# Kernel optimization log

Measured on AMD Instinct MI355X. Metric: run time of the kernel, lower is better.

## Reference

```python
import jax, jax.numpy as jnp
import numpy as np

B, N, NIN = 32, 128, 64
MSG_HID, MSG_OUT, N_HID, N_OUT = 256, 64, 256, 64
E = N * (N - 1)  # fully connected, no self loops


def setup_inputs() -> dict:
    key = jax.random.key(0)
    ks = jax.random.split(key, 12)

    # one-hot incidence matrices (NRI convention)
    off = np.ones((N, N), dtype=np.float32) - np.eye(N, dtype=np.float32)
    recv_idx, send_idx = np.where(off)
    eye = np.eye(N, dtype=np.float32)
    rel_rec = jnp.asarray(eye[recv_idx])    # [E, N]
    rel_send = jnp.asarray(eye[send_idx])   # [E, N]

    s = 0.05
    inp = {
        "inputs": jax.random.normal(ks[0], (B, N, NIN), jnp.float32),
        "rel_rec": rel_rec,
        "rel_send": rel_send,
        "rel_types": jax.random.uniform(ks[1], (B, E, 2), jnp.float32),
        "msg_fc1_w": jax.random.normal(ks[2], (MSG_HID, 2 * NIN), jnp.float32) * s,
        "msg_fc1_b": jnp.zeros((MSG_HID,), jnp.float32),
        "msg_fc2_w": jax.random.normal(ks[3], (MSG_OUT, MSG_HID), jnp.float32) * s,
        "msg_fc2_b": jnp.zeros((MSG_OUT,), jnp.float32),
        "out_fc1_w": jax.random.normal(ks[4], (N_HID, MSG_OUT), jnp.float32) * s,
        "out_fc1_b": jnp.zeros((N_HID,), jnp.float32),
        "out_fc2_w": jax.random.normal(ks[5], (N_HID, N_HID), jnp.float32) * s,
        "out_fc2_b": jnp.zeros((N_HID,), jnp.float32),
        "out_fc3_w": jax.random.normal(ks[6], (N_OUT, N_HID), jnp.float32) * s,
        "out_fc3_b": jnp.zeros((N_OUT,), jnp.float32),
    }
    return inp


def reference(inputs, rel_rec, rel_send, rel_types,
              msg_fc1_w, msg_fc1_b, msg_fc2_w, msg_fc2_b,
              out_fc1_w, out_fc1_b, out_fc2_w, out_fc2_b,
              out_fc3_w, out_fc3_b):
    # node2edge: gather sender / receiver node features via one-hot matmul
    senders = jnp.einsum('en,bnf->bef', rel_send, inputs)    # [B,E,NIN]
    receivers = jnp.einsum('en,bnf->bef', rel_rec, inputs)   # [B,E,NIN]
    pre_msg = jnp.concatenate([senders, receivers], axis=-1)  # [B,E,2*NIN]

    all_msgs = jnp.zeros(pre_msg.shape[:2] + (MSG_OUT,), pre_msg.dtype)
    for i in range(2):  # edge-type loop (shared weights, as in the original)
        msg = jax.nn.relu(pre_msg @ msg_fc1_w.T + msg_fc1_b)
        msg = jax.nn.relu(msg @ msg_fc2_w.T + msg_fc2_b)
        all_msgs = all_msgs + msg * rel_types[:, :, i:i + 1]

    # edge2node: scatter-add messages to receiving nodes
    agg_msgs = jnp.einsum('bem,en->bnm', all_msgs, rel_rec)   # [B,N,MSG_OUT]

    pred = jax.nn.relu(agg_msgs @ out_fc1_w.T + out_fc1_b)
    pred = jax.nn.relu(pred @ out_fc2_w.T + out_fc2_b)
    pred = pred @ out_fc3_w.T + out_fc3_b                      # [B,N,N_OUT]
    return pred
```

## Files before the change

kernel.cpp:

```cpp
#include <hip/hip_runtime.h>

#define BB 32
#define NN_ 128
#define NIN 64
#define MH 256
#define MO 64
#define NH 256
#define NO 64
#define EDGES 16256

typedef __attribute__((ext_vector_type(8))) short short8;
typedef __attribute__((ext_vector_type(4))) float f32x4;


static __device__ __forceinline__ unsigned short f2bf(float f) {
    unsigned u = __float_as_uint(f);
    u = (u + 0x7fffu + ((u >> 16) & 1u)) >> 16;
    return (unsigned short)u;
}

static __device__ __forceinline__ unsigned bf_pack(float lo, float hi) {
    return __builtin_amdgcn_perm(__float_as_uint(hi) + 0x8000u,
                                 __float_as_uint(lo) + 0x8000u, 0x07060302u);
}

__global__ __launch_bounds__(256) void prep_kernel(
    const float* __restrict__ x, const float* __restrict__ W1,
    const float* __restrict__ b1, const float* __restrict__ W2,
    const float* __restrict__ O1, const float* __restrict__ O2,
    const float* __restrict__ O3,
    unsigned short* __restrict__ psb, unsigned short* __restrict__ prb,
    unsigned short* __restrict__ w2b, unsigned short* __restrict__ o1b,
    unsigned short* __restrict__ o2b, unsigned short* __restrict__ o3b)
{
    int blk = blockIdx.x;
    int t = threadIdx.x;
    if (blk < 1024) {
        int b  = blk >> 5;
        int n0 = (blk & 31) << 2;
        __shared__ float xL[4][64];
        xL[t >> 6][t & 63] = x[((b * NN_) + n0 + (t >> 6)) * NIN + (t & 63)];
        __syncthreads();

        const float4* w1r = (const float4*)(W1 + t * (2 * NIN));
        float psv[4] = {0.f, 0.f, 0.f, 0.f};
        float prv[4];
        float bv = b1[t];
        #pragma unroll
        for (int nn = 0; nn < 4; ++nn) prv[nn] = bv;

        #pragma unroll
        for (int f4 = 0; f4 < 16; ++f4) {
            float4 w = w1r[f4];
            #pragma unroll
            for (int nn = 0; nn < 4; ++nn)
                psv[nn] += w.x * xL[nn][4*f4+0] + w.y * xL[nn][4*f4+1]
                         + w.z * xL[nn][4*f4+2] + w.w * xL[nn][4*f4+3];
        }
        #pragma unroll
        for (int f4 = 0; f4 < 16; ++f4) {
            float4 w = w1r[16 + f4];
            #pragma unroll
            for (int nn = 0; nn < 4; ++nn)
                prv[nn] += w.x * xL[nn][4*f4+0] + w.y * xL[nn][4*f4+1]
                         + w.z * xL[nn][4*f4+2] + w.w * xL[nn][4*f4+3];
        }
        #pragma unroll
        for (int nn = 0; nn < 4; ++nn) {
            int n = n0 + nn;
            prb[((b * NN_) + n) * MH + t] = f2bf(prv[nn]);
            psb[(((b * 32) + (t >> 3)) * NN_ + n) * 8 + (t & 7)] = f2bf(psv[nn]);
        }
    } else if (blk < 1088) {
        int i = ((blk - 1024) << 8) + t;
        int kc4 = i >> 9, rem = i & 511;
        int n = rem >> 3, k7 = i & 7;
        int k = kc4 * 8 + k7;
        w2b[i] = f2bf(W2[n * MH + k]);
    } else {
        int i = ((blk - 1088) << 8) + t;
        if (i < 16384)       o1b[i]         = f2bf(O1[i]);
        else if (i < 81920)  o2b[i - 16384] = f2bf(O2[i - 16384]);
        else                 o3b[i - 81920] = f2bf(O3[i - 81920]);
    }
}

__global__ __launch_bounds__(256, 4) void edge_kernel(
    const float* __restrict__ rt, const float* __restrict__ b2,
    const unsigned short* __restrict__ psb, const unsigned short* __restrict__ prb,
    const unsigned short* __restrict__ w2b, float* __restrict__ agg)
{
    int blk = blockIdx.x;
    int b = blk >> 7;
    int r = blk & 127;
    int tid = threadIdx.x;
    int w = tid >> 6;
    int lane = tid & 63;
    int ml = lane & 15;
    int q  = lane >> 4;

    __shared__ float rtw_lds[128];
    __shared__ float red[4][64];
    if (tid < 128) {
        float v = 0.f;
        if (tid < 127) {
            const float* p = rt + ((size_t)(b * EDGES + r * 127 + tid)) * 2;
            v = p[0] + p[1];
        }
        rtw_lds[tid] = v;
    }
    __syncthreads();

    int slot0 = 32 * w + ml;
    int slot1 = slot0 + 16;
    int snd0 = slot0 + (slot0 >= r ? 1 : 0); if (snd0 > 127) snd0 = 127;
    int snd1 = slot1 + (slot1 >= r ? 1 : 0); if (snd1 > 127) snd1 = 127;

    const uint4* ps4 = (const uint4*)psb + (size_t)b * (32 * NN_);
    const uint4* pr4 = (const uint4*)(prb + ((size_t)(b * NN_ + r)) * MH);
    const uint4* w24 = (const uint4*)w2b;

    f32x4 acc[2][4];
    #pragma unroll
    for (int mt = 0; mt < 2; ++mt)
        #pragma unroll
        for (int nt = 0; nt < 4; ++nt)
            acc[mt][nt] = (f32x4){0.f, 0.f, 0.f, 0.f};

    #pragma unroll
    for (int kc = 0; kc < 8; ++kc) {
        int kc4 = 4 * kc + q;
        uint4 upr = pr4[kc4];
        uint4 us0 = ps4[kc4 * NN_ + snd0];
        uint4 us1 = ps4[kc4 * NN_ + snd1];

        float plo[4], phi[4];
        plo[0] = __uint_as_float(upr.x << 16); phi[0] = __uint_as_float(upr.x & 0xffff0000u);
        plo[1] = __uint_as_float(upr.y << 16); phi[1] = __uint_as_float(upr.y & 0xffff0000u);
        plo[2] = __uint_as_float(upr.z << 16); phi[2] = __uint_as_float(upr.z & 0xffff0000u);
        plo[3] = __uint_as_float(upr.w << 16); phi[3] = __uint_as_float(upr.w & 0xffff0000u);

        uint4 a0u, a1u;
        {
            unsigned c;
            c = us0.x; a0u.x = bf_pack(fmaxf(__uint_as_float(c << 16) + plo[0], 0.f),
                                       fmaxf(__uint_as_float(c & 0xffff0000u) + phi[0], 0.f));
            c = us0.y; a0u.y = bf_pack(fmaxf(__uint_as_float(c << 16) + plo[1], 0.f),
                                       fmaxf(__uint_as_float(c & 0xffff0000u) + phi[1], 0.f));
            c = us0.z; a0u.z = bf_pack(fmaxf(__uint_as_float(c << 16) + plo[2], 0.f),
                                       fmaxf(__uint_as_float(c & 0xffff0000u) + phi[2], 0.f));
            c = us0.w; a0u.w = bf_pack(fmaxf(__uint_as_float(c << 16) + plo[3], 0.f),
                                       fmaxf(__uint_as_float(c & 0xffff0000u) + phi[3], 0.f));
            c = us1.x; a1u.x = bf_pack(fmaxf(__uint_as_float(c << 16) + plo[0], 0.f),
                                       fmaxf(__uint_as_float(c & 0xffff0000u) + phi[0], 0.f));
            c = us1.y; a1u.y = bf_pack(fmaxf(__uint_as_float(c << 16) + plo[1], 0.f),
                                       fmaxf(__uint_as_float(c & 0xffff0000u) + phi[1], 0.f));
            c = us1.z; a1u.z = bf_pack(fmaxf(__uint_as_float(c << 16) + plo[2], 0.f),
                                       fmaxf(__uint_as_float(c & 0xffff0000u) + phi[2], 0.f));
            c = us1.w; a1u.w = bf_pack(fmaxf(__uint_as_float(c << 16) + plo[3], 0.f),
                                       fmaxf(__uint_as_float(c & 0xffff0000u) + phi[3], 0.f));
        }
        short8 a0 = __builtin_bit_cast(short8, a0u);
        short8 a1 = __builtin_bit_cast(short8, a1u);

        #pragma unroll
        for (int nt = 0; nt < 4; ++nt) {
            uint4 uw = w24[kc4 * 64 + 16 * nt + ml];
            short8 bf = __builtin_bit_cast(short8, uw);
            acc[0][nt] = __builtin_amdgcn_mfma_f32_16x16x32_bf16(a0, bf, acc[0][nt], 0, 0, 0);
            acc[1][nt] = __builtin_amdgcn_mfma_f32_16x16x32_bf16(a1, bf, acc[1][nt], 0, 0, 0);
        }
    }

    float b2c[4];
    #pragma unroll
    for (int nt = 0; nt < 4; ++nt) b2c[nt] = b2[16 * nt + ml];

    float colsum[4] = {0.f, 0.f, 0.f, 0.f};
    #pragma unroll
    for (int mt = 0; mt < 2; ++mt) {
        int slotbase = 32 * w + 16 * mt + 4 * q;
        #pragma unroll
        for (int reg = 0; reg < 4; ++reg) {
            float rw = rtw_lds[slotbase + reg];
            #pragma unroll
            for (int nt = 0; nt < 4; ++nt)
                colsum[nt] += fmaxf(acc[mt][nt][reg] + b2c[nt], 0.f) * rw;
        }
    }
    #pragma unroll
    for (int nt = 0; nt < 4; ++nt) {
        colsum[nt] += __shfl_xor(colsum[nt], 16);
        colsum[nt] += __shfl_xor(colsum[nt], 32);
    }
    if (lane < 16) {
        #pragma unroll
        for (int nt = 0; nt < 4; ++nt) red[w][16 * nt + ml] = colsum[nt];
    }
    __syncthreads();
    if (tid < 64)
        agg[((size_t)(b * NN_ + r)) * MO + tid] =
            red[0][tid] + red[1][tid] + red[2][tid] + red[3][tid];
}

__global__ __launch_bounds__(256) void node_kernel(
    const float* __restrict__ agg,
    const unsigned short* __restrict__ O1b, const float* __restrict__ b1o,
    const unsigned short* __restrict__ O2b, const float* __restrict__ b2o,
    const unsigned short* __restrict__ O3b, const float* __restrict__ b3o,
    float* __restrict__ out)
{
    int tid = threadIdx.x;
    int w = tid >> 6, lane = tid & 63, ml = lane & 15, q = lane >> 4;
    int row0 = blockIdx.x << 4;

    __shared__ unsigned short h1L[16][264];
    __shared__ unsigned short h2L[16][264];

    short8 aA[2];
    #pragma unroll
    for (int s = 0; s < 2; ++s) {
        const float* base = agg + (size_t)(row0 + ml) * MO + 32 * s + q * 8;
        float4 f0 = *(const float4*)base;
        float4 f1 = *(const float4*)(base + 4);
        uint4 u;
        u.x = bf_pack(f0.x, f0.y);
        u.y = bf_pack(f0.z, f0.w);
        u.z = bf_pack(f1.x, f1.y);
        u.w = bf_pack(f1.z, f1.w);
        aA[s] = __builtin_bit_cast(short8, u);
    }

    #pragma unroll
    for (int nt = 0; nt < 4; ++nt) {
        int ntg = w * 4 + nt;
        f32x4 acc = (f32x4){0.f, 0.f, 0.f, 0.f};
        #pragma unroll
        for (int s = 0; s < 2; ++s) {
            uint4 uw = *(const uint4*)(O1b + (size_t)(ntg * 16 + ml) * 64 + 32 * s + q * 8);
            acc = __builtin_amdgcn_mfma_f32_16x16x32_bf16(
                aA[s], __builtin_bit_cast(short8, uw), acc, 0, 0, 0);
        }
        float bv = b1o[ntg * 16 + ml];
        #pragma unroll
        for (int reg = 0; reg < 4; ++reg)
            h1L[q * 4 + reg][ntg * 16 + ml] = f2bf(fmaxf(acc[reg] + bv, 0.f));
    }
    __syncthreads();

    short8 aH[8];
    #pragma unroll
    for (int ks = 0; ks < 8; ++ks)
        aH[ks] = *(const short8*)&h1L[ml][32 * ks + q * 8];
    #pragma unroll
    for (int nt = 0; nt < 4; ++nt) {
        int ntg = w * 4 + nt;
        const unsigned short* wrow = O2b + (size_t)(ntg * 16 + ml) * NH + q * 8;
        f32x4 acc = (f32x4){0.f, 0.f, 0.f, 0.f};
        #pragma unroll
        for (int ks = 0; ks < 8; ++ks) {
            uint4 uw = *(const uint4*)(wrow + 32 * ks);
            acc = __builtin_amdgcn_mfma_f32_16x16x32_bf16(
                aH[ks], __builtin_bit_cast(short8, uw), acc, 0, 0, 0);
        }
        float bv = b2o[ntg * 16 + ml];
        #pragma unroll
        for (int reg = 0; reg < 4; ++reg)
            h2L[q * 4 + reg][ntg * 16 + ml] = f2bf(fmaxf(acc[reg] + bv, 0.f));
    }
    __syncthreads();

    #pragma unroll
    for (int ks = 0; ks < 8; ++ks)
        aH[ks] = *(const short8*)&h2L[ml][32 * ks + q * 8];
    {
        const unsigned short* wrow = O3b + (size_t)(w * 16 + ml) * NH + q * 8;
        f32x4 acc = (f32x4){0.f, 0.f, 0.f, 0.f};
        #pragma unroll
        for (int ks = 0; ks < 8; ++ks) {
            uint4 uw = *(const uint4*)(wrow + 32 * ks);
            acc = __builtin_amdgcn_mfma_f32_16x16x32_bf16(
                aH[ks], __builtin_bit_cast(short8, uw), acc, 0, 0, 0);
        }
        float bv = b3o[w * 16 + ml];
        #pragma unroll
        for (int reg = 0; reg < 4; ++reg)
            out[(size_t)(row0 + q * 4 + reg) * NO + w * 16 + ml] = acc[reg] + bv;
    }
}

extern "C" void kernel_launch(void* const* d_in, const int* in_sizes, int n_in,
                              void* d_out, int out_size, void* d_ws, size_t ws_size,
                              hipStream_t stream) {
    const float* x   = (const float*)d_in[0];
    const float* rt  = (const float*)d_in[3];
    const float* W1  = (const float*)d_in[4];
    const float* b1  = (const float*)d_in[5];
    const float* W2  = (const float*)d_in[6];
    const float* b2  = (const float*)d_in[7];
    const float* O1  = (const float*)d_in[8];
    const float* b1o = (const float*)d_in[9];
    const float* O2  = (const float*)d_in[10];
    const float* b2o = (const float*)d_in[11];
    const float* O3  = (const float*)d_in[12];
    const float* b3o = (const float*)d_in[13];

    float* ws  = (float*)d_ws;
    unsigned short* psb = (unsigned short*)ws;
    unsigned short* prb = (unsigned short*)(ws + 524288);
    unsigned short* w2b = (unsigned short*)(ws + 1048576);
    float* agg = ws + 1056768;
    unsigned short* o1b = (unsigned short*)(ws + 1318912);
    unsigned short* o2b = (unsigned short*)(ws + 1327104);
    unsigned short* o3b = (unsigned short*)(ws + 1359872);
    float* out = (float*)d_out;

    hipLaunchKernelGGL(prep_kernel, dim3(1472), dim3(256), 0, stream,
                       x, W1, b1, W2, O1, O2, O3, psb, prb, w2b, o1b, o2b, o3b);
    hipLaunchKernelGGL(edge_kernel, dim3(4096), dim3(256), 0, stream,
                       rt, b2, psb, prb, w2b, agg);
    hipLaunchKernelGGL(node_kernel, dim3(256), dim3(256), 0, stream,
                       agg, o1b, b1o, o2b, b2o, o3b, b3o, out);
}
```

Baseline: 152.6 us.

## Process two receivers per edge block and use MFMA for node projection

The edge kernel now handles two receiver nodes per block. Each sender-feature load and each W2 fragment load is reused across both receivers, and the grid is halved. Senders are indexed directly, with the self edge given zero weight, which drops the per-receiver index remapping. The prep kernel replaces the scalar FP32 W1 projection with bf16 MFMA tiles over 16 node rows, converting W1 on the fly. The price is more accumulator registers in the edge kernel (launch bound lowered to 3 waves) and extra rounding of W1 to bf16.

```diff
diff --git a/kernel.cpp b/kernel.cpp
--- a/kernel.cpp
+++ b/kernel.cpp
@@ -22,6 +22,31 @@
 static __device__ __forceinline__ unsigned bf_pack(float lo, float hi) {
     return __builtin_amdgcn_perm(__float_as_uint(hi) + 0x8000u,
                                  __float_as_uint(lo) + 0x8000u, 0x07060302u);
+}
+
+static __device__ __forceinline__ short8 pack8(float4 f0, float4 f1) {
+    uint4 u;
+    u.x = bf_pack(f0.x, f0.y);
+    u.y = bf_pack(f0.z, f0.w);
+    u.z = bf_pack(f1.x, f1.y);
+    u.w = bf_pack(f1.z, f1.w);
+    return __builtin_bit_cast(short8, u);
+}
+
+static __device__ __forceinline__ void unpack8(uint4 u, float* f) {
+    f[0] = __uint_as_float(u.x << 16); f[1] = __uint_as_float(u.x & 0xffff0000u);
+    f[2] = __uint_as_float(u.y << 16); f[3] = __uint_as_float(u.y & 0xffff0000u);
+    f[4] = __uint_as_float(u.z << 16); f[5] = __uint_as_float(u.z & 0xffff0000u);
+    f[6] = __uint_as_float(u.w << 16); f[7] = __uint_as_float(u.w & 0xffff0000u);
+}
+
+static __device__ __forceinline__ short8 buildA(const float* s, const float* p) {
+    uint4 u;
+    u.x = bf_pack(fmaxf(s[0] + p[0], 0.f), fmaxf(s[1] + p[1], 0.f));
+    u.y = bf_pack(fmaxf(s[2] + p[2], 0.f), fmaxf(s[3] + p[3], 0.f));
+    u.z = bf_pack(fmaxf(s[4] + p[4], 0.f), fmaxf(s[5] + p[5], 0.f));
+    u.w = bf_pack(fmaxf(s[6] + p[6], 0.f), fmaxf(s[7] + p[7], 0.f));
+    return __builtin_bit_cast(short8, u);
 }
 
 __global__ __launch_bounds__(256) void prep_kernel(
@@ -35,140 +60,128 @@
 {
     int blk = blockIdx.x;
     int t = threadIdx.x;
-    if (blk < 1024) {
-        int b  = blk >> 5;
-        int n0 = (blk & 31) << 2;
-        __shared__ float xL[4][64];
-        xL[t >> 6][t & 63] = x[((b * NN_) + n0 + (t >> 6)) * NIN + (t & 63)];
-        __syncthreads();
-
-        const float4* w1r = (const float4*)(W1 + t * (2 * NIN));
-        float psv[4] = {0.f, 0.f, 0.f, 0.f};
-        float prv[4];
-        float bv = b1[t];
-        #pragma unroll
-        for (int nn = 0; nn < 4; ++nn) prv[nn] = bv;
-
-        #pragma unroll
-        for (int f4 = 0; f4 < 16; ++f4) {
-            float4 w = w1r[f4];
+    if (blk < 256) {
+        int row0 = blk << 4;
+        int b = blk >> 3;
+        int w = t >> 6, lane = t & 63, ml = lane & 15, q = lane >> 4;
+
+        short8 aX[2];
+        #pragma unroll
+        for (int s = 0; s < 2; ++s) {
+            const float* base = x + (size_t)(row0 + ml) * NIN + s * 32 + q * 8;
+            aX[s] = pack8(*(const float4*)base, *(const float4*)(base + 4));
+        }
+
+        #pragma unroll
+        for (int half = 0; half < 2; ++half) {
             #pragma unroll
-            for (int nn = 0; nn < 4; ++nn)
-                psv[nn] += w.x * xL[nn][4*f4+0] + w.y * xL[nn][4*f4+1]
-                         + w.z * xL[nn][4*f4+2] + w.w * xL[nn][4*f4+3];
-        }
-        #pragma unroll
-        for (int f4 = 0; f4 < 16; ++f4) {
-            float4 w = w1r[16 + f4];
-            #pragma unroll
-            for (int nn = 0; nn < 4; ++nn)
-                prv[nn] += w.x * xL[nn][4*f4+0] + w.y * xL[nn][4*f4+1]
-                         + w.z * xL[nn][4*f4+2] + w.w * xL[nn][4*f4+3];
-        }
-        #pragma unroll
-        for (int nn = 0; nn < 4; ++nn) {
-            int n = n0 + nn;
-            prb[((b * NN_) + n) * MH + t] = f2bf(prv[nn]);
-            psb[(((b * 32) + (t >> 3)) * NN_ + n) * 8 + (t & 7)] = f2bf(psv[nn]);
-        }
-    } else if (blk < 1088) {
-        int i = ((blk - 1024) << 8) + t;
+            for (int nt = 0; nt < 4; ++nt) {
+                int col = w * 64 + nt * 16 + ml;
+                const float* wrow = W1 + (size_t)col * (2 * NIN) + half * 64 + q * 8;
+                f32x4 acc = (f32x4){0.f, 0.f, 0.f, 0.f};
+                #pragma unroll
+                for (int s = 0; s < 2; ++s) {
+                    short8 bw = pack8(*(const float4*)(wrow + 32 * s),
+                                      *(const float4*)(wrow + 32 * s + 4));
+                    acc = __builtin_amdgcn_mfma_f32_16x16x32_bf16(aX[s], bw, acc, 0, 0, 0);
+                }
+                if (half == 0) {
+                    #pragma unroll
+                    for (int reg = 0; reg < 4; ++reg) {
+                        int n = (row0 + q * 4 + reg) & 127;
+                        psb[((size_t)(b * 32 + (col >> 3)) * NN_ + n) * 8 + (col & 7)]
+                            = f2bf(acc[reg]);
+                    }
+                } else {
+                    float bv = b1[col];
+                    #pragma unroll
+                    for (int reg = 0; reg < 4; ++reg) {
+                        int n = (row0 + q * 4 + reg) & 127;
+                        prb[((size_t)(b * NN_) + n) * MH + col] = f2bf(acc[reg] + bv);
+                    }
+                }
+            }
+        }
+    } else if (blk < 320) {
+        int i = ((blk - 256) << 8) + t;
         int kc4 = i >> 9, rem = i & 511;
         int n = rem >> 3, k7 = i & 7;
-        int k = kc4 * 8 + k7;
-        w2b[i] = f2bf(W2[n * MH + k]);
+        w2b[i] = f2bf(W2[n * MH + kc4 * 8 + k7]);
     } else {
-        int i = ((blk - 1088) << 8) + t;
+        int i = ((blk - 320) << 8) + t;
         if (i < 16384)       o1b[i]         = f2bf(O1[i]);
         else if (i < 81920)  o2b[i - 16384] = f2bf(O2[i - 16384]);
         else                 o3b[i - 81920] = f2bf(O3[i - 81920]);
     }
 }
 
-__global__ __launch_bounds__(256, 4) void edge_kernel(
+__global__ __launch_bounds__(256, 3) void edge_kernel(
     const float* __restrict__ rt, const float* __restrict__ b2,
     const unsigned short* __restrict__ psb, const unsigned short* __restrict__ prb,
     const unsigned short* __restrict__ w2b, float* __restrict__ agg)
 {
     int blk = blockIdx.x;
-    int b = blk >> 7;
-    int r = blk & 127;
+    int b = blk >> 6;
+    int r0 = (blk & 63) << 1;
     int tid = threadIdx.x;
-    int w = tid >> 6;
-    int lane = tid & 63;
-    int ml = lane & 15;
-    int q  = lane >> 4;
-
-    __shared__ float rtw_lds[128];
-    __shared__ float red[4][64];
-    if (tid < 128) {
+    int w = tid >> 6, lane = tid & 63, ml = lane & 15, q = lane >> 4;
+
+    __shared__ float rtw_lds[2][128];
+    __shared__ float red[2][4][64];
+    {
+        int rr = tid >> 7, s = tid & 127;
+        int r = r0 + rr;
         float v = 0.f;
-        if (tid < 127) {
-            const float* p = rt + ((size_t)(b * EDGES + r * 127 + tid)) * 2;
+        if (s != r) {
+            int e = r * 127 + s - (s > r ? 1 : 0);
+            const float* p = rt + ((size_t)(b * EDGES + e)) * 2;
             v = p[0] + p[1];
         }
-        rtw_lds[tid] = v;
+        rtw_lds[rr][s] = v;
     }
     __syncthreads();
 
     int slot0 = 32 * w + ml;
     int slot1 = slot0 + 16;
-    int snd0 = slot0 + (slot0 >= r ? 1 : 0); if (snd0 > 127) snd0 = 127;
-    int snd1 = slot1 + (slot1 >= r ? 1 : 0); if (snd1 > 127) snd1 = 127;
 
     const uint4* ps4 = (const uint4*)psb + (size_t)b * (32 * NN_);
-    const uint4* pr4 = (const uint4*)(prb + ((size_t)(b * NN_ + r)) * MH);
+    const uint4* pr4_0 = (const uint4*)(prb + ((size_t)(b * NN_ + r0)) * MH);
+    const uint4* pr4_1 = (const uint4*)(prb + ((size_t)(b * NN_ + r0 + 1)) * MH);
     const uint4* w24 = (const uint4*)w2b;
 
-    f32x4 acc[2][4];
-    #pragma unroll
-    for (int mt = 0; mt < 2; ++mt)
-        #pragma unroll
-        for (int nt = 0; nt < 4; ++nt)
-            acc[mt][nt] = (f32x4){0.f, 0.f, 0.f, 0.f};
+    f32x4 acc[2][2][4];
+    #pragma unroll
+    for (int rr = 0; rr < 2; ++rr)
+        #pragma unroll
+        for (int mt = 0; mt < 2; ++mt)
+            #pragma unroll
+            for (int nt = 0; nt < 4; ++nt)
+                acc[rr][mt][nt] = (f32x4){0.f, 0.f, 0.f, 0.f};
 
     #pragma unroll
     for (int kc = 0; kc < 8; ++kc) {
         int kc4 = 4 * kc + q;
-        uint4 upr = pr4[kc4];
-        uint4 us0 = ps4[kc4 * NN_ + snd0];
-        uint4 us1 = ps4[kc4 * NN_ + snd1];
-
-        float plo[4], phi[4];
-        plo[0] = __uint_as_float(upr.x << 16); phi[0] = __uint_as_float(upr.x & 0xffff0000u);
-        plo[1] = __uint_as_float(upr.y << 16); phi[1] = __uint_as_float(upr.y & 0xffff0000u);
-        plo[2] = __uint_as_float(upr.z << 16); phi[2] = __uint_as_float(upr.z & 0xffff0000u);
-        plo[3] = __uint_as_float(upr.w << 16); phi[3] = __uint_as_float(upr.w & 0xffff0000u);
-
-        uint4 a0u, a1u;
-        {
-            unsigned c;
-            c = us0.x; a0u.x = bf_pack(fmaxf(__uint_as_float(c << 16) + plo[0], 0.f),
-                                       fmaxf(__uint_as_float(c & 0xffff0000u) + phi[0], 0.f));
-            c = us0.y; a0u.y = bf_pack(fmaxf(__uint_as_float(c << 16) + plo[1], 0.f),
-                                       fmaxf(__uint_as_float(c & 0xffff0000u) + phi[1], 0.f));
-            c = us0.z; a0u.z = bf_pack(fmaxf(__uint_as_float(c << 16) + plo[2], 0.f),
-                                       fmaxf(__uint_as_float(c & 0xffff0000u) + phi[2], 0.f));
-            c = us0.w; a0u.w = bf_pack(fmaxf(__uint_as_float(c << 16) + plo[3], 0.f),
-                                       fmaxf(__uint_as_float(c & 0xffff0000u) + phi[3], 0.f));
-            c = us1.x; a1u.x = bf_pack(fmaxf(__uint_as_float(c << 16) + plo[0], 0.f),
-                                       fmaxf(__uint_as_float(c & 0xffff0000u) + phi[0], 0.f));
-            c = us1.y; a1u.y = bf_pack(fmaxf(__uint_as_float(c << 16) + plo[1], 0.f),
-                                       fmaxf(__uint_as_float(c & 0xffff0000u) + phi[1], 0.f));
-            c = us1.z; a1u.z = bf_pack(fmaxf(__uint_as_float(c << 16) + plo[2], 0.f),
-                                       fmaxf(__uint_as_float(c & 0xffff0000u) + phi[2], 0.f));
-            c = us1.w; a1u.w = bf_pack(fmaxf(__uint_as_float(c << 16) + plo[3], 0.f),
-                                       fmaxf(__uint_as_float(c & 0xffff0000u) + phi[3], 0.f));
-        }
-        short8 a0 = __builtin_bit_cast(short8, a0u);
-        short8 a1 = __builtin_bit_cast(short8, a1u);
+        uint4 us0 = ps4[kc4 * NN_ + slot0];
+        uint4 us1 = ps4[kc4 * NN_ + slot1];
+        uint4 up0 = pr4_0[kc4];
+        uint4 up1 = pr4_1[kc4];
+
+        float s0f[8], s1f[8], p0f[8], p1f[8];
+        unpack8(us0, s0f); unpack8(us1, s1f);
+        unpack8(up0, p0f); unpack8(up1, p1f);
+
+        short8 a00 = buildA(s0f, p0f);
+        short8 a01 = buildA(s1f, p0f);
+        short8 a10 = buildA(s0f, p1f);
+        short8 a11 = buildA(s1f, p1f);
 
         #pragma unroll
         for (int nt = 0; nt < 4; ++nt) {
-            uint4 uw = w24[kc4 * 64 + 16 * nt + ml];
-            short8 bf = __builtin_bit_cast(short8, uw);
-            acc[0][nt] = __builtin_amdgcn_mfma_f32_16x16x32_bf16(a0, bf, acc[0][nt], 0, 0, 0);
-            acc[1][nt] = __builtin_amdgcn_mfma_f32_16x16x32_bf16(a1, bf, acc[1][nt], 0, 0, 0);
+            short8 bw = __builtin_bit_cast(short8, w24[kc4 * 64 + 16 * nt + ml]);
+            acc[0][0][nt] = __builtin_amdgcn_mfma_f32_16x16x32_bf16(a00, bw, acc[0][0][nt], 0, 0, 0);
+            acc[0][1][nt] = __builtin_amdgcn_mfma_f32_16x16x32_bf16(a01, bw, acc[0][1][nt], 0, 0, 0);
+            acc[1][0][nt] = __builtin_amdgcn_mfma_f32_16x16x32_bf16(a10, bw, acc[1][0][nt], 0, 0, 0);
+            acc[1][1][nt] = __builtin_amdgcn_mfma_f32_16x16x32_bf16(a11, bw, acc[1][1][nt], 0, 0, 0);
         }
     }
 
@@ -176,31 +189,36 @@
     #pragma unroll
     for (int nt = 0; nt < 4; ++nt) b2c[nt] = b2[16 * nt + ml];
 
-    float colsum[4] = {0.f, 0.f, 0.f, 0.f};
-    #pragma unroll
-    for (int mt = 0; mt < 2; ++mt) {
-        int slotbase = 32 * w + 16 * mt + 4 * q;
-        #pragma unroll
-        for (int reg = 0; reg < 4; ++reg) {
-            float rw = rtw_lds[slotbase + reg];
+    #pragma unroll
+    for (int rr = 0; rr < 2; ++rr) {
+        float colsum[4] = {0.f, 0.f, 0.f, 0.f};
+        #pragma unroll
+        for (int mt = 0; mt < 2; ++mt) {
+            int slotbase = 32 * w + 16 * mt + 4 * q;
             #pragma unroll
-            for (int nt = 0; nt < 4; ++nt)
-                colsum[nt] += fmaxf(acc[mt][nt][reg] + b2c[nt], 0.f) * rw;
-        }
-    }
-    #pragma unroll
-    for (int nt = 0; nt < 4; ++nt) {
-        colsum[nt] += __shfl_xor(colsum[nt], 16);
-        colsum[nt] += __shfl_xor(colsum[nt], 32);
-    }
-    if (lane < 16) {
-        #pragma unroll
-        for (int nt = 0; nt < 4; ++nt) red[w][16 * nt + ml] = colsum[nt];
+            for (int reg = 0; reg < 4; ++reg) {
+                float rw = rtw_lds[rr][slotbase + reg];
+                #pragma unroll
+                for (int nt = 0; nt < 4; ++nt)
+                    colsum[nt] += fmaxf(acc[rr][mt][nt][reg] + b2c[nt], 0.f) * rw;
+            }
+        }
+        #pragma unroll
+        for (int nt = 0; nt < 4; ++nt) {
+            colsum[nt] += __shfl_xor(colsum[nt], 16);
+            colsum[nt] += __shfl_xor(colsum[nt], 32);
+        }
+        if (lane < 16) {
+            #pragma unroll
+            for (int nt = 0; nt < 4; ++nt) red[rr][w][16 * nt + ml] = colsum[nt];
+        }
     }
     __syncthreads();
-    if (tid < 64)
-        agg[((size_t)(b * NN_ + r)) * MO + tid] =
-            red[0][tid] + red[1][tid] + red[2][tid] + red[3][tid];
+    if (tid < 128) {
+        int rr = tid >> 6, o = tid & 63;
+        agg[((size_t)(b * NN_ + r0 + rr)) * MO + o] =
+            red[rr][0][o] + red[rr][1][o] + red[rr][2][o] + red[rr][3][o];
+    }
 }
 
 __global__ __launch_bounds__(256) void node_kernel(
@@ -221,14 +239,7 @@
     #pragma unroll
     for (int s = 0; s < 2; ++s) {
         const float* base = agg + (size_t)(row0 + ml) * MO + 32 * s + q * 8;
-        float4 f0 = *(const float4*)base;
-        float4 f1 = *(const float4*)(base + 4);
-        uint4 u;
-        u.x = bf_pack(f0.x, f0.y);
-        u.y = bf_pack(f0.z, f0.w);
-        u.z = bf_pack(f1.x, f1.y);
-        u.w = bf_pack(f1.z, f1.w);
-        aA[s] = __builtin_bit_cast(short8, u);
+        aA[s] = pack8(*(const float4*)base, *(const float4*)(base + 4));
     }
 
     #pragma unroll
@@ -315,9 +326,9 @@
     unsigned short* o3b = (unsigned short*)(ws + 1359872);
     float* out = (float*)d_out;
 
-    hipLaunchKernelGGL(prep_kernel, dim3(1472), dim3(256), 0, stream,
+    hipLaunchKernelGGL(prep_kernel, dim3(704), dim3(256), 0, stream,
                        x, W1, b1, W2, O1, O2, O3, psb, prb, w2b, o1b, o2b, o3b);
-    hipLaunchKernelGGL(edge_kernel, dim3(4096), dim3(256), 0, stream,
+    hipLaunchKernelGGL(edge_kernel, dim3(2048), dim3(256), 0, stream,
                        rt, b2, psb, prb, w2b, agg);
     hipLaunchKernelGGL(node_kernel, dim3(256), dim3(256), 0, stream,
                        agg, o1b, b1o, o2b, b2o, o3b, b3o, out);
```

After: 130.3 us. -14.6%, faster.
